# Optimization experiments

Hardware: AMD Instinct MI355X
Metric: run time of the kernel (lower is better)

The kernel has to match this reference:

```python
import jax, jax.numpy as jnp
import numpy as np

N = 262144
D_IN = 128
ENC_DIMS = [128, 512, 256, 64, 8]   # input -> hidden tanh layers -> linear latent
EST_DIMS = [8, 128, 64, 16]          # latent -> hidden tanh layers -> softmax K
EPS = 1e-6


def setup_inputs() -> dict:
    key = jax.random.key(0)
    ks = jax.random.split(key, 1 + 2 * (len(ENC_DIMS) - 1) + 2 * (len(EST_DIMS) - 1))
    it = iter(ks)
    inp = {"x": jax.random.normal(next(it), (N, D_IN), dtype=jnp.float32)}
    for i in range(len(ENC_DIMS) - 1):
        fan_in, fan_out = ENC_DIMS[i], ENC_DIMS[i + 1]
        inp[f"W{i}"] = jax.random.normal(next(it), (fan_in, fan_out), dtype=jnp.float32) * (1.0 / np.sqrt(fan_in))
        inp[f"b{i}"] = jnp.zeros((fan_out,), dtype=jnp.float32)
    for i in range(len(EST_DIMS) - 1):
        fan_in, fan_out = EST_DIMS[i], EST_DIMS[i + 1]
        inp[f"E{i}"] = jax.random.normal(next(it), (fan_in, fan_out), dtype=jnp.float32) * (1.0 / np.sqrt(fan_in))
        inp[f"eb{i}"] = jnp.zeros((fan_out,), dtype=jnp.float32)
    return inp


def _forward(x, W0, b0, W1, b1, W2, b2, W3, b3, E0, eb0, E1, eb1, E2, eb2):
    # CompressionNet encoder: tanh hidden layers, linear final
    h = jnp.tanh(x @ W0 + b0)
    h = jnp.tanh(h @ W1 + b1)
    h = jnp.tanh(h @ W2 + b2)
    z = h @ W3 + b3                                  # [N, d_z]

    # EstimationNet: tanh hidden layers, softmax final -> gamma [N, K]
    g = jnp.tanh(z @ E0 + eb0)
    g = jnp.tanh(g @ E1 + eb1)
    gamma = jax.nn.softmax(g @ E2 + eb2, axis=1)

    # GMM statistics
    gamma_sum = jnp.sum(gamma, axis=0)               # [K]
    phi = jnp.mean(gamma, axis=0)                    # [K]
    mu = (gamma.T @ z) / gamma_sum[:, None]          # [K, d_z]
    zc_raw = z[:, None, :] - mu[None, :, :]          # [N, K, d_z]
    zc = jnp.sqrt(gamma)[:, :, None] * zc_raw        # [N, K, d_z]
    sigma = jnp.einsum('nkl,nkm->klm', zc, zc) / gamma_sum[:, None, None]  # [K, d, d]
    d_z = z.shape[1]
    L = jnp.linalg.cholesky(sigma + EPS * jnp.eye(d_z, dtype=sigma.dtype)[None])

    # Energy: solve L v = (z - mu)^T per component, [K, d, N]
    v = jax.scipy.linalg.solve_triangular(L, jnp.transpose(zc_raw, (1, 2, 0)), lower=True)
    log_det_sigma = 2.0 * jnp.sum(jnp.log(jnp.diagonal(L, axis1=1, axis2=2)), axis=1)  # [K]
    logits = (jnp.log(phi)[:, None]
              - 0.5 * (jnp.sum(v * v, axis=1)
                       + d_z * jnp.log(2.0 * jnp.pi)
                       + log_det_sigma[:, None]))    # [K, N]
    prob = -jax.scipy.special.logsumexp(logits, axis=0)  # [N]
    return prob, z


def reference(x, W0, b0, W1, b1, W2, b2, W3, b3, E0, eb0, E1, eb1, E2, eb2):
    return _forward(x, W0, b0, W1, b1, W2, b2, W3, b3, E0, eb0, E1, eb1, E2, eb2)
```

## Files before the change

### kernel.cpp

```cpp
#include <hip/hip_runtime.h>
#include <math.h>

#define NSAMP 262144
#define TMS 64

typedef __bf16  bf16x8 __attribute__((ext_vector_type(8)));
typedef __bf16  bf16x4 __attribute__((ext_vector_type(4)));
typedef float   f32x4  __attribute__((ext_vector_type(4)));

__device__ __forceinline__ float fast_tanh(float v) {
  float e = __expf(2.0f * v);
  return 1.0f - 2.0f * __builtin_amdgcn_rcpf(e + 1.0f);
}
__device__ __forceinline__ unsigned short f2bf(float f) {
  unsigned u = __float_as_uint(f);
  unsigned r = (u + 0x7FFFu + ((u >> 16) & 1u)) >> 16;
  return (unsigned short)r;
}

__global__ void k0_pack(const float* __restrict__ W0, const float* __restrict__ W1,
                        const float* __restrict__ W2, const float* __restrict__ E1w,
                        const float* __restrict__ E0w, const float* __restrict__ W3,
                        const float* __restrict__ E2w,
                        unsigned short* __restrict__ wpack)
{
  const int f = blockIdx.x;
  const int lane = threadIdx.x;
  const float* W; int NKS, N, Kreal, Nreal, local;
  if (f < 128)      { W = W0;  NKS = 4;  N = 512; Kreal = 128; Nreal = 512; local = f; }
  else if (f < 384) { W = W1;  NKS = 16; N = 256; Kreal = 512; Nreal = 256; local = f - 128; }
  else if (f < 416) { W = W2;  NKS = 8;  N = 64;  Kreal = 256; Nreal = 64;  local = f - 384; }
  else if (f < 432) { W = E1w; NKS = 4;  N = 64;  Kreal = 128; Nreal = 64;  local = f - 416; }
  else if (f < 440) { W = E0w; NKS = 1;  N = 128; Kreal = 8;   Nreal = 128; local = f - 432; }
  else if (f < 442) { W = W3;  NKS = 2;  N = 8;   Kreal = 64;  Nreal = 8;   local = f - 440; }
  else              { W = E2w; NKS = 2;  N = 16;  Kreal = 64;  Nreal = 16;  local = f - 442; }
  const int nt = local / NKS, ks = local % NKS;
  const int n = nt * 16 + (lane & 15);
  const int kbase = ks * 32 + (lane >> 4) * 8;
  unsigned short* out = wpack + ((size_t)f * 64 + lane) * 8;
#pragma unroll
  for (int i = 0; i < 8; ++i) {
    const int k = kbase + i;
    const float v = (k < Kreal && n < Nreal) ? W[(size_t)k * N + n] : 0.f;
    out[i] = f2bf(v);
  }
}

template<int NTPW>
__device__ __forceinline__ void layer_nks4(
    const char* __restrict__ in, int inRowB, char* __restrict__ outb, int outRowB,
    const unsigned short* __restrict__ wp, int fragBase,
    const float* __restrict__ bias, int lane, int wv)
{
  const int l15 = lane & 15, lg = lane >> 4;
  const int sw = (l15 & 7) << 4;
  bf16x8 a[4][4];
#pragma unroll
  for (int sg = 0; sg < 4; ++sg)
#pragma unroll
    for (int q = 0; q < 4; ++q)
      a[sg][q] = *(const bf16x8*)(in + (sg * 16 + l15) * inRowB + ((q * 64 + lg * 16) ^ sw));
#pragma unroll
  for (int t = 0; t < NTPW; ++t) {
    const int nt = wv * NTPW + t;
    const float4 bv = *(const float4*)(bias + nt * 16 + lg * 4);
    f32x4 acc[4];
#pragma unroll
    for (int sg = 0; sg < 4; ++sg) acc[sg] = {bv.x, bv.y, bv.z, bv.w};
#pragma unroll
    for (int q = 0; q < 4; ++q) {
      const bf16x8 w = *(const bf16x8*)(wp + ((size_t)(fragBase + nt * 4 + q) * 64 + lane) * 8);
#pragma unroll
      for (int sg = 0; sg < 4; ++sg)
        acc[sg] = __builtin_amdgcn_mfma_f32_16x16x32_bf16(w, a[sg][q], acc[sg], 0, 0, 0);
    }
#pragma unroll
    for (int sg = 0; sg < 4; ++sg) {
      bf16x4 tv;
#pragma unroll
      for (int r = 0; r < 4; ++r) tv[r] = (__bf16)fast_tanh(acc[sg][r]);
      *(bf16x4*)(outb + (sg * 16 + l15) * outRowB + ((nt * 32 + lg * 8) ^ sw)) = tv;
    }
  }
}

template<int NCH>
__device__ __forceinline__ void l2_accum(
    const char* __restrict__ H1, const unsigned short* __restrict__ wp,
    int ksOff, f32x4 (&acc)[4][4], int lane, int wv)
{
  const int l15 = lane & 15, lg = lane >> 4;
  const int sw = (l15 & 7) << 4;
#pragma unroll
  for (int ch = 0; ch < NCH; ++ch) {
    bf16x8 a[4][4];
#pragma unroll
    for (int sg = 0; sg < 4; ++sg)
#pragma unroll
      for (int q = 0; q < 4; ++q)
        a[sg][q] = *(const bf16x8*)(H1 + (sg * 16 + l15) * 512 + (((ch * 4 + q) * 64 + lg * 16) ^ sw));
#pragma unroll
    for (int t = 0; t < 4; ++t) {
      const int nt = wv * 4 + t;
#pragma unroll
      for (int q = 0; q < 4; ++q) {
        const bf16x8 w = *(const bf16x8*)(wp + ((size_t)(128 + nt * 16 + ksOff + ch * 4 + q) * 64 + lane) * 8);
#pragma unroll
        for (int sg = 0; sg < 4; ++sg)
          acc[t][sg] = __builtin_amdgcn_mfma_f32_16x16x32_bf16(w, a[sg][q], acc[t][sg], 0, 0, 0);
      }
    }
  }
}

__global__ __launch_bounds__(256, 2) void k1_mfma(
    const float* __restrict__ x, const unsigned short* __restrict__ wpack,
    const float* __restrict__ b0, const float* __restrict__ b1,
    const float* __restrict__ b2, const float* __restrict__ b3,
    const float* __restrict__ eb0, const float* __restrict__ eb1,
    const float* __restrict__ eb2,
    float* __restrict__ zg, float* __restrict__ gamma)
{
  __shared__ char sm[81920];
  char* H1  = sm;
  char* H2  = sm + 32768;
  char* X   = sm + 65536;
  char* L3o = sm + 65536;
  char* zb  = sm + 73728;
  char* E0o = sm;
  char* e1  = sm + 32768;

  const int tid = threadIdx.x;
  const int lane = tid & 63, wv = tid >> 6;
  const int l15 = lane & 15, lg = lane >> 4;
  const int sw = (l15 & 7) << 4;
  const int blk = blockIdx.x;

  {
    const float* xb = x + (size_t)blk * (TMS * 128);
#pragma unroll
    for (int p = 0; p < 8; ++p) {
      const int v = tid + p * 256;
      const float4 t = *(const float4*)(xb + v * 4);
      const int s = v >> 5, k0 = (v & 31) * 4;
      bf16x4 h = {(__bf16)t.x, (__bf16)t.y, (__bf16)t.z, (__bf16)t.w};
      *(bf16x4*)(X + s * 256 + ((k0 * 2) ^ ((s & 7) << 4))) = h;
    }
  }

  f32x4 acc2[4][4];
#pragma unroll
  for (int t = 0; t < 4; ++t) {
    const float4 bv = *(const float4*)(b1 + (wv * 4 + t) * 16 + lg * 4);
#pragma unroll
    for (int sg = 0; sg < 4; ++sg) acc2[t][sg] = {bv.x, bv.y, bv.z, bv.w};
  }
  __syncthreads();

  layer_nks4<4>(X, 256, H1, 512, wpack, 0, b0, lane, wv);
  __syncthreads();
  l2_accum<2>(H1, wpack, 0, acc2, lane, wv);
  __syncthreads();
  layer_nks4<4>(X, 256, H1, 512, wpack, 64, b0 + 256, lane, wv);
  __syncthreads();
  l2_accum<2>(H1, wpack, 8, acc2, lane, wv);

#pragma unroll
  for (int t = 0; t < 4; ++t)
#pragma unroll
    for (int sg = 0; sg < 4; ++sg) {
      bf16x4 tv;
#pragma unroll
      for (int r = 0; r < 4; ++r) tv[r] = (__bf16)fast_tanh(acc2[t][sg][r]);
      *(bf16x4*)(H2 + (sg * 16 + l15) * 512 + (((wv * 4 + t) * 32 + lg * 8) ^ sw)) = tv;
    }
  __syncthreads();

  {
    f32x4 acc[4];
    const float4 bv = *(const float4*)(b2 + wv * 16 + lg * 4);
#pragma unroll
    for (int sg = 0; sg < 4; ++sg) acc[sg] = {bv.x, bv.y, bv.z, bv.w};
#pragma unroll
    for (int ch = 0; ch < 2; ++ch) {
      bf16x8 a[4][4];
#pragma unroll
      for (int sg = 0; sg < 4; ++sg)
#pragma unroll
        for (int q = 0; q < 4; ++q)
          a[sg][q] = *(const bf16x8*)(H2 + (sg * 16 + l15) * 512 + (((ch * 4 + q) * 64 + lg * 16) ^ sw));
#pragma unroll
      for (int q = 0; q < 4; ++q) {
        const bf16x8 w = *(const bf16x8*)(wpack + ((size_t)(384 + wv * 8 + ch * 4 + q) * 64 + lane) * 8);
#pragma unroll
        for (int sg = 0; sg < 4; ++sg)
          acc[sg] = __builtin_amdgcn_mfma_f32_16x16x32_bf16(w, a[sg][q], acc[sg], 0, 0, 0);
      }
    }
#pragma unroll
    for (int sg = 0; sg < 4; ++sg) {
      bf16x4 tv;
#pragma unroll
      for (int r = 0; r < 4; ++r) tv[r] = (__bf16)fast_tanh(acc[sg][r]);
      *(bf16x4*)(L3o + (sg * 16 + l15) * 128 + ((wv * 32 + lg * 8) ^ sw)) = tv;
    }
  }
  __syncthreads();

  {
    bf16x8 a[2];
#pragma unroll
    for (int q = 0; q < 2; ++q)
      a[q] = *(const bf16x8*)(L3o + (wv * 16 + l15) * 128 + ((q * 64 + lg * 16) ^ sw));
    float4 bv = {0.f, 0.f, 0.f, 0.f};
    if (lg < 2) bv = *(const float4*)(b3 + lg * 4);
    f32x4 acc = {bv.x, bv.y, bv.z, bv.w};
#pragma unroll
    for (int q = 0; q < 2; ++q) {
      const bf16x8 w = *(const bf16x8*)(wpack + ((size_t)(440 + q) * 64 + lane) * 8);
      acc = __builtin_amdgcn_mfma_f32_16x16x32_bf16(w, a[q], acc, 0, 0, 0);
    }
    if (lg < 2) {
      *(f32x4*)(zg + ((size_t)blk * 64 + wv * 16 + l15) * 8 + lg * 4) = acc;
      bf16x4 zv;
#pragma unroll
      for (int r = 0; r < 4; ++r) zv[r] = (__bf16)acc[r];
      *(bf16x4*)(zb + (wv * 16 + l15) * 16 + lg * 8) = zv;
    }
  }
  __syncthreads();

  {
    bf16x8 az[4];
#pragma unroll
    for (int sg = 0; sg < 4; ++sg)
      az[sg] = *(const bf16x8*)(zb + (sg * 16 + l15) * 16);
#pragma unroll
    for (int t = 0; t < 2; ++t) {
      const int nt = wv * 2 + t;
      const float4 bv = *(const float4*)(eb0 + nt * 16 + lg * 4);
      const bf16x8 w = *(const bf16x8*)(wpack + ((size_t)(432 + nt) * 64 + lane) * 8);
#pragma unroll
      for (int sg = 0; sg < 4; ++sg) {
        f32x4 acc = {bv.x, bv.y, bv.z, bv.w};
        acc = __builtin_amdgcn_mfma_f32_16x16x32_bf16(w, az[sg], acc, 0, 0, 0);
        bf16x4 tv;
#pragma unroll
        for (int r = 0; r < 4; ++r) tv[r] = (__bf16)fast_tanh(acc[r]);
        *(bf16x4*)(E0o + (sg * 16 + l15) * 256 + ((nt * 32 + lg * 8) ^ sw)) = tv;
      }
    }
  }
  __syncthreads();

  layer_nks4<1>(E0o, 256, e1, 128, wpack, 416, eb1, lane, wv);
  __syncthreads();

  {
    bf16x8 a[2];
#pragma unroll
    for (int q = 0; q < 2; ++q)
      a[q] = *(const bf16x8*)(e1 + (wv * 16 + l15) * 128 + ((q * 64 + lg * 16) ^ sw));
    const float4 bv = *(const float4*)(eb2 + lg * 4);
    f32x4 acc = {bv.x, bv.y, bv.z, bv.w};
#pragma unroll
    for (int q = 0; q < 2; ++q) {
      const bf16x8 w = *(const bf16x8*)(wpack + ((size_t)(442 + q) * 64 + lane) * 8);
      acc = __builtin_amdgcn_mfma_f32_16x16x32_bf16(w, a[q], acc, 0, 0, 0);
    }
    float m = fmaxf(fmaxf(acc[0], acc[1]), fmaxf(acc[2], acc[3]));
    m = fmaxf(m, __shfl_xor(m, 16));
    m = fmaxf(m, __shfl_xor(m, 32));
    float e0v = __expf(acc[0] - m), e1v = __expf(acc[1] - m);
    float e2v = __expf(acc[2] - m), e3v = __expf(acc[3] - m);
    float s = e0v + e1v + e2v + e3v;
    s += __shfl_xor(s, 16);
    s += __shfl_xor(s, 32);
    const float inv = __builtin_amdgcn_rcpf(s);
    float4 g = {e0v * inv, e1v * inv, e2v * inv, e3v * inv};
    *(float4*)(gamma + ((size_t)blk * 64 + wv * 16 + l15) * 16 + lg * 4) = g;
  }
}

__global__ __launch_bounds__(256) void k2a_partial(
    const float* __restrict__ zg, const float* __restrict__ gamma,
    float* __restrict__ part)
{
  __shared__ float zl[256 * 8];
  __shared__ float gl[256 * 16];
  __shared__ float red[4][16][46];
  const int tid = threadIdx.x;
  const int blk = blockIdx.x;
  const int s0 = blk * 256;

  {
    const float4 a = *(const float4*)(zg + (size_t)(s0 + tid) * 8);
    const float4 b = *(const float4*)(zg + (size_t)(s0 + tid) * 8 + 4);
    *(float4*)(&zl[tid * 8])     = a;
    *(float4*)(&zl[tid * 8 + 4]) = b;
  }
  {
    const float* gp = gamma + (size_t)(s0 + tid) * 16;
#pragma unroll
    for (int q = 0; q < 4; ++q)
      *(float4*)(&gl[tid * 16 + q * 4]) = *(const float4*)(gp + q * 4);
  }
  __syncthreads();

  const int k = tid & 15, sub = tid >> 4;
  float m2[36], m1[8], gs = 0.f;
#pragma unroll
  for (int i = 0; i < 36; ++i) m2[i] = 0.f;
#pragma unroll
  for (int i = 0; i < 8; ++i) m1[i] = 0.f;

#pragma unroll 4
  for (int i = 0; i < 16; ++i) {
    const int n = i * 16 + sub;
    const float4 za = *(const float4*)(&zl[n * 8]);
    const float4 zb4 = *(const float4*)(&zl[n * 8 + 4]);
    const float zv[8] = {za.x, za.y, za.z, za.w, zb4.x, zb4.y, zb4.z, zb4.w};
    const float g = gl[n * 16 + k];
    gs += g;
    float t[8];
#pragma unroll
    for (int l = 0; l < 8; ++l) { t[l] = g * zv[l]; m1[l] += t[l]; }
    int p = 0;
#pragma unroll
    for (int l = 0; l < 8; ++l)
#pragma unroll
      for (int m = l; m < 8; ++m) {
        m2[p] = fmaf(t[l], zv[m], m2[p]);
        ++p;
      }
  }

#pragma unroll
  for (int i = 0; i < 36; ++i) {
    m2[i] += __shfl_xor(m2[i], 16);
    m2[i] += __shfl_xor(m2[i], 32);
  }
#pragma unroll
  for (int i = 0; i < 8; ++i) {
    m1[i] += __shfl_xor(m1[i], 16);
    m1[i] += __shfl_xor(m1[i], 32);
  }
  gs += __shfl_xor(gs, 16);
  gs += __shfl_xor(gs, 32);

  const int lane = tid & 63, wv = tid >> 6;
  if (lane < 16) {
#pragma unroll
    for (int i = 0; i < 36; ++i) red[wv][lane][i] = m2[i];
#pragma unroll
    for (int i = 0; i < 8; ++i) red[wv][lane][36 + i] = m1[i];
    red[wv][lane][44] = gs;
  }
  __syncthreads();

  for (int o = tid; o < 768; o += 256) {
    const int kk = o / 48, p = o % 48;
    float v = 0.f;
    if (p < 45)
      v = red[0][kk][p] + red[1][kk][p] + red[2][kk][p] + red[3][kk][p];
    part[(size_t)blk * 768 + o] = v;
  }
}

__global__ __launch_bounds__(256) void k2b_reduce(
    const float* __restrict__ part, float* __restrict__ stats)
{
  const int oi = blockIdx.x % 3, jc = blockIdx.x / 3;
  const int o = oi * 256 + threadIdx.x;
  float s = 0.f;
#pragma unroll 4
  for (int j = jc * 128; j < jc * 128 + 128; ++j)
    s += part[(size_t)j * 768 + o];
  atomicAdd(&stats[o], s);
}

__global__ void k3_finalize(const float* __restrict__ stats, float* __restrict__ coef)
{
  const int k = threadIdx.x;
  if (k >= 16) return;
  const float* sk = stats + k * 48;
  const float gs = sk[44];
  float mu[8];
#pragma unroll
  for (int l = 0; l < 8; ++l) mu[l] = sk[36 + l] / gs;

  float S[8][8];
  {
    int p = 0;
    for (int l = 0; l < 8; ++l)
      for (int m = l; m < 8; ++m) {
        const float v = sk[p++] / gs - mu[l] * mu[m];
        S[l][m] = v; S[m][l] = v;
      }
  }
  for (int l = 0; l < 8; ++l) S[l][l] += 1e-6f;

  float L[8][8];
  for (int i = 0; i < 8; ++i)
    for (int j = 0; j <= i; ++j) {
      float s = S[i][j];
      for (int t = 0; t < j; ++t) s -= L[i][t] * L[j][t];
      if (i == j) L[i][i] = sqrtf(s);
      else        L[i][j] = s / L[j][j];
    }
  float logdet = 0.f;
  for (int i = 0; i < 8; ++i) logdet += logf(L[i][i]);
  logdet *= 2.f;

  float U[8][8];
  for (int j = 0; j < 8; ++j) {
    U[j][j] = 1.f / L[j][j];
    for (int i = j + 1; i < 8; ++i) {
      float s = 0.f;
      for (int t = j; t < i; ++t) s += L[i][t] * U[t][j];
      U[i][j] = -s / L[i][i];
    }
  }
  float Amat[8][8];
  for (int l = 0; l < 8; ++l)
    for (int m = l; m < 8; ++m) {
      float s = 0.f;
      for (int i = m; i < 8; ++i) s += U[i][l] * U[i][m];
      Amat[l][m] = s; Amat[m][l] = s;
    }
  float c[8];
  for (int l = 0; l < 8; ++l) {
    float s = 0.f;
    for (int m = 0; m < 8; ++m) s += Amat[l][m] * mu[m];
    c[l] = s;
  }
  float muAmu = 0.f;
  for (int l = 0; l < 8; ++l) muAmu += c[l] * mu[l];

  const float LOG2PI = 1.8378770664093453f;
  const float cnst = logf(gs) - logf((float)NSAMP)
                   - 0.5f * (8.f * LOG2PI + logdet + muAmu);

  float* ck = coef + k * 48;
  {
    int p = 0;
    for (int l = 0; l < 8; ++l)
      for (int m = l; m < 8; ++m) {
        ck[p] = (l == m) ? (-0.5f * Amat[l][l]) : (-Amat[l][m]);
        ++p;
      }
  }
  for (int l = 0; l < 8; ++l) ck[36 + l] = c[l];
  ck[44] = cnst;
  ck[45] = 0.f; ck[46] = 0.f; ck[47] = 0.f;
}

__global__ __launch_bounds__(256) void k4_energy(
    const float* __restrict__ zg, const float* __restrict__ coef,
    float* __restrict__ prob)
{
  __shared__ float C[16 * 48];
  for (int i = threadIdx.x; i < 16 * 48; i += 256) C[i] = coef[i];
  __syncthreads();

  const int n = blockIdx.x * 256 + threadIdx.x;
  const float4 za = *(const float4*)(zg + (size_t)n * 8);
  const float4 zb = *(const float4*)(zg + (size_t)n * 8 + 4);
  const float z[8] = {za.x, za.y, za.z, za.w, zb.x, zb.y, zb.z, zb.w};

  float pr[36];
  {
    int p = 0;
#pragma unroll
    for (int l = 0; l < 8; ++l)
#pragma unroll
      for (int m = l; m < 8; ++m) pr[p++] = z[l] * z[m];
  }

  float mx = -1e30f, sm = 0.f;
#pragma unroll
  for (int k = 0; k < 16; ++k) {
    const float4* c4 = (const float4*)&C[k * 48];
    float acc = C[k * 48 + 44];
#pragma unroll
    for (int q = 0; q < 9; ++q) {
      const float4 t = c4[q];
      acc = fmaf(t.x, pr[q * 4 + 0], acc);
      acc = fmaf(t.y, pr[q * 4 + 1], acc);
      acc = fmaf(t.z, pr[q * 4 + 2], acc);
      acc = fmaf(t.w, pr[q * 4 + 3], acc);
    }
    {
      const float4 t = c4[9];
      acc = fmaf(t.x, z[0], acc); acc = fmaf(t.y, z[1], acc);
      acc = fmaf(t.z, z[2], acc); acc = fmaf(t.w, z[3], acc);
    }
    {
      const float4 t = c4[10];
      acc = fmaf(t.x, z[4], acc); acc = fmaf(t.y, z[5], acc);
      acc = fmaf(t.z, z[6], acc); acc = fmaf(t.w, z[7], acc);
    }
    const float nm = fmaxf(mx, acc);
    sm = sm * __expf(mx - nm) + __expf(acc - nm);
    mx = nm;
  }
  prob[n] = -(mx + __logf(sm));
}

extern "C" void kernel_launch(void* const* d_in, const int* in_sizes, int n_in,
                              void* d_out, int out_size, void* d_ws, size_t ws_size,
                              hipStream_t stream)
{
  const float* x   = (const float*)d_in[0];
  const float* W0  = (const float*)d_in[1];
  const float* b0  = (const float*)d_in[2];
  const float* W1  = (const float*)d_in[3];
  const float* b1  = (const float*)d_in[4];
  const float* W2  = (const float*)d_in[5];
  const float* b2  = (const float*)d_in[6];
  const float* W3  = (const float*)d_in[7];
  const float* b3  = (const float*)d_in[8];
  const float* E0w = (const float*)d_in[9];
  const float* eb0 = (const float*)d_in[10];
  const float* E1w = (const float*)d_in[11];
  const float* eb1 = (const float*)d_in[12];
  const float* E2w = (const float*)d_in[13];
  const float* eb2 = (const float*)d_in[14];

  float* out  = (float*)d_out;
  float* prob = out;
  float* zg   = out + NSAMP;

  unsigned short* wpack = (unsigned short*)d_ws;
  float* ws    = (float*)d_ws;
  float* gamma = ws + 114688;
  float* stats = gamma + (size_t)NSAMP * 16;
  float* coef  = stats + 768;
  float* part  = coef + 768;

  hipMemsetAsync(stats, 0, 768 * sizeof(float), stream);

  k0_pack<<<444, 64, 0, stream>>>(W0, W1, W2, E1w, E0w, W3, E2w, wpack);
  k1_mfma<<<NSAMP / TMS, 256, 0, stream>>>(x, wpack, b0, b1, b2, b3,
                                           eb0, eb1, eb2, zg, gamma);
  k2a_partial<<<1024, 256, 0, stream>>>(zg, gamma, part);
  k2b_reduce<<<24, 256, 0, stream>>>(part, stats);
  k3_finalize<<<1, 64, 0, stream>>>(stats, coef);
  k4_energy<<<NSAMP / 256, 256, 0, stream>>>(zg, coef, prob);
}
```

Before: 204.4 us.

## Fuse GMM partial statistics into MLP kernel and shrink shared memory footprint

The per-sample gamma write and the separate k2a_partial kernel are removed. Each k1 block now reduces the GMM moment statistics for its 64 samples in shared memory and writes partials directly. Layer 1/2 processing is split into four 128-wide chunks and layer 3 into two halves, cutting LDS use from 80KB to 48KB so occupancy can rise to 3 blocks per CU. This saves a 16MB gamma round trip and one launch. In exchange, k2b now reduces four times more partials, and k1 has more barriers and higher register pressure.

Measured after the change: 301.8 us. 1.48x slower.

```diff
diff --git a/kernel.cpp b/kernel.cpp
--- a/kernel.cpp
+++ b/kernel.cpp
@@ -84,51 +84,67 @@
   }
 }
 
-template<int NCH>
-__device__ __forceinline__ void l2_accum(
+__device__ __forceinline__ void l2_accum_q(
     const char* __restrict__ H1, const unsigned short* __restrict__ wp,
     int ksOff, f32x4 (&acc)[4][4], int lane, int wv)
 {
   const int l15 = lane & 15, lg = lane >> 4;
   const int sw = (l15 & 7) << 4;
-#pragma unroll
-  for (int ch = 0; ch < NCH; ++ch) {
-    bf16x8 a[4][4];
-#pragma unroll
-    for (int sg = 0; sg < 4; ++sg)
-#pragma unroll
-      for (int q = 0; q < 4; ++q)
-        a[sg][q] = *(const bf16x8*)(H1 + (sg * 16 + l15) * 512 + (((ch * 4 + q) * 64 + lg * 16) ^ sw));
-#pragma unroll
-    for (int t = 0; t < 4; ++t) {
-      const int nt = wv * 4 + t;
-#pragma unroll
-      for (int q = 0; q < 4; ++q) {
-        const bf16x8 w = *(const bf16x8*)(wp + ((size_t)(128 + nt * 16 + ksOff + ch * 4 + q) * 64 + lane) * 8);
-#pragma unroll
-        for (int sg = 0; sg < 4; ++sg)
-          acc[t][sg] = __builtin_amdgcn_mfma_f32_16x16x32_bf16(w, a[sg][q], acc[t][sg], 0, 0, 0);
-      }
-    }
-  }
-}
-
-__global__ __launch_bounds__(256, 2) void k1_mfma(
+  bf16x8 a[4][4];
+#pragma unroll
+  for (int sg = 0; sg < 4; ++sg)
+#pragma unroll
+    for (int q = 0; q < 4; ++q)
+      a[sg][q] = *(const bf16x8*)(H1 + (sg * 16 + l15) * 256 + ((q * 64 + lg * 16) ^ sw));
+#pragma unroll
+  for (int t = 0; t < 4; ++t) {
+    const int nt = wv * 4 + t;
+#pragma unroll
+    for (int q = 0; q < 4; ++q) {
+      const bf16x8 w = *(const bf16x8*)(wp + ((size_t)(128 + nt * 16 + ksOff + q) * 64 + lane) * 8);
+#pragma unroll
+      for (int sg = 0; sg < 4; ++sg)
+        acc[t][sg] = __builtin_amdgcn_mfma_f32_16x16x32_bf16(w, a[sg][q], acc[t][sg], 0, 0, 0);
+    }
+  }
+}
+
+__device__ __forceinline__ void l3_accum_h(
+    const char* __restrict__ H2, const unsigned short* __restrict__ wp,
+    int ksOff, f32x4 (&acc)[4], int lane, int wv)
+{
+  const int l15 = lane & 15, lg = lane >> 4;
+  const int sw = (l15 & 7) << 4;
+#pragma unroll
+  for (int q = 0; q < 4; ++q) {
+    const bf16x8 w = *(const bf16x8*)(wp + ((size_t)(384 + wv * 8 + ksOff + q) * 64 + lane) * 8);
+#pragma unroll
+    for (int sg = 0; sg < 4; ++sg) {
+      const bf16x8 a = *(const bf16x8*)(H2 + (sg * 16 + l15) * 256 + ((q * 64 + lg * 16) ^ sw));
+      acc[sg] = __builtin_amdgcn_mfma_f32_16x16x32_bf16(w, a, acc[sg], 0, 0, 0);
+    }
+  }
+}
+
+__global__ __launch_bounds__(256, 3) void k1_mfma(
     const float* __restrict__ x, const unsigned short* __restrict__ wpack,
     const float* __restrict__ b0, const float* __restrict__ b1,
     const float* __restrict__ b2, const float* __restrict__ b3,
     const float* __restrict__ eb0, const float* __restrict__ eb1,
     const float* __restrict__ eb2,
-    float* __restrict__ zg, float* __restrict__ gamma)
-{
-  __shared__ char sm[81920];
-  char* H1  = sm;
+    float* __restrict__ zg, float* __restrict__ part)
+{
+  __shared__ char sm[49152];
+  char* X   = sm;
+  char* H1  = sm + 16384;
   char* H2  = sm + 32768;
-  char* X   = sm + 65536;
-  char* L3o = sm + 65536;
-  char* zb  = sm + 73728;
-  char* E0o = sm;
+  char* L3o = sm;
+  float* zf = (float*)(sm + 8192);
+  char* zb  = sm + 10240;
+  float* gl = (float*)(sm + 11264);
+  char* E0o = sm + 16384;
   char* e1  = sm + 32768;
+  float (*red)[16][46] = (float(*)[16][46])(sm + 16384);
 
   const int tid = threadIdx.x;
   const int lane = tid & 63, wv = tid >> 6;
@@ -157,53 +173,58 @@
   }
   __syncthreads();
 
-  layer_nks4<4>(X, 256, H1, 512, wpack, 0, b0, lane, wv);
-  __syncthreads();
-  l2_accum<2>(H1, wpack, 0, acc2, lane, wv);
-  __syncthreads();
-  layer_nks4<4>(X, 256, H1, 512, wpack, 64, b0 + 256, lane, wv);
-  __syncthreads();
-  l2_accum<2>(H1, wpack, 8, acc2, lane, wv);
-
-#pragma unroll
-  for (int t = 0; t < 4; ++t)
-#pragma unroll
-    for (int sg = 0; sg < 4; ++sg) {
-      bf16x4 tv;
-#pragma unroll
-      for (int r = 0; r < 4; ++r) tv[r] = (__bf16)fast_tanh(acc2[t][sg][r]);
-      *(bf16x4*)(H2 + (sg * 16 + l15) * 512 + (((wv * 4 + t) * 32 + lg * 8) ^ sw)) = tv;
-    }
-  __syncthreads();
-
-  {
-    f32x4 acc[4];
+#pragma unroll
+  for (int p = 0; p < 4; ++p) {
+    layer_nks4<2>(X, 256, H1, 256, wpack, p * 32, b0 + p * 128, lane, wv);
+    __syncthreads();
+    l2_accum_q(H1, wpack, p * 4, acc2, lane, wv);
+    __syncthreads();
+  }
+
+  f32x4 acc3[4];
+  {
     const float4 bv = *(const float4*)(b2 + wv * 16 + lg * 4);
 #pragma unroll
-    for (int sg = 0; sg < 4; ++sg) acc[sg] = {bv.x, bv.y, bv.z, bv.w};
-#pragma unroll
-    for (int ch = 0; ch < 2; ++ch) {
-      bf16x8 a[4][4];
-#pragma unroll
-      for (int sg = 0; sg < 4; ++sg)
-#pragma unroll
-        for (int q = 0; q < 4; ++q)
-          a[sg][q] = *(const bf16x8*)(H2 + (sg * 16 + l15) * 512 + (((ch * 4 + q) * 64 + lg * 16) ^ sw));
-#pragma unroll
-      for (int q = 0; q < 4; ++q) {
-        const bf16x8 w = *(const bf16x8*)(wpack + ((size_t)(384 + wv * 8 + ch * 4 + q) * 64 + lane) * 8);
-#pragma unroll
-        for (int sg = 0; sg < 4; ++sg)
-          acc[sg] = __builtin_amdgcn_mfma_f32_16x16x32_bf16(w, a[sg][q], acc[sg], 0, 0, 0);
+    for (int sg = 0; sg < 4; ++sg) acc3[sg] = {bv.x, bv.y, bv.z, bv.w};
+  }
+
+  if (wv < 2) {
+#pragma unroll
+    for (int t = 0; t < 4; ++t)
+#pragma unroll
+      for (int sg = 0; sg < 4; ++sg) {
+        bf16x4 tv;
+#pragma unroll
+        for (int r = 0; r < 4; ++r) tv[r] = (__bf16)fast_tanh(acc2[t][sg][r]);
+        const int tl = wv * 4 + t;
+        *(bf16x4*)(H2 + (sg * 16 + l15) * 256 + ((tl * 32 + lg * 8) ^ sw)) = tv;
       }
-    }
-#pragma unroll
-    for (int sg = 0; sg < 4; ++sg) {
-      bf16x4 tv;
-#pragma unroll
-      for (int r = 0; r < 4; ++r) tv[r] = (__bf16)fast_tanh(acc[sg][r]);
-      *(bf16x4*)(L3o + (sg * 16 + l15) * 128 + ((wv * 32 + lg * 8) ^ sw)) = tv;
-    }
+  }
+  __syncthreads();
+  l3_accum_h(H2, wpack, 0, acc3, lane, wv);
+  __syncthreads();
+
+  if (wv >= 2) {
+#pragma unroll
+    for (int t = 0; t < 4; ++t)
+#pragma unroll
+      for (int sg = 0; sg < 4; ++sg) {
+        bf16x4 tv;
+#pragma unroll
+        for (int r = 0; r < 4; ++r) tv[r] = (__bf16)fast_tanh(acc2[t][sg][r]);
+        const int tl = (wv - 2) * 4 + t;
+        *(bf16x4*)(H2 + (sg * 16 + l15) * 256 + ((tl * 32 + lg * 8) ^ sw)) = tv;
+      }
+  }
+  __syncthreads();
+  l3_accum_h(H2, wpack, 4, acc3, lane, wv);
+
+#pragma unroll
+  for (int sg = 0; sg < 4; ++sg) {
+    bf16x4 tv;
+#pragma unroll
+    for (int r = 0; r < 4; ++r) tv[r] = (__bf16)fast_tanh(acc3[sg][r]);
+    *(bf16x4*)(L3o + (sg * 16 + l15) * 128 + ((wv * 32 + lg * 8) ^ sw)) = tv;
   }
   __syncthreads();
 
@@ -222,6 +243,7 @@
     }
     if (lg < 2) {
       *(f32x4*)(zg + ((size_t)blk * 64 + wv * 16 + l15) * 8 + lg * 4) = acc;
+      *(f32x4*)(zf + (wv * 16 + l15) * 8 + lg * 4) = acc;
       bf16x4 zv;
 #pragma unroll
       for (int r = 0; r < 4; ++r) zv[r] = (__bf16)acc[r];
@@ -277,84 +299,57 @@
     s += __shfl_xor(s, 16);
     s += __shfl_xor(s, 32);
     const float inv = __builtin_amdgcn_rcpf(s);
-    float4 g = {e0v * inv, e1v * inv, e2v * inv, e3v * inv};
-    *(float4*)(gamma + ((size_t)blk * 64 + wv * 16 + l15) * 16 + lg * 4) = g;
-  }
-}
-
-__global__ __launch_bounds__(256) void k2a_partial(
-    const float* __restrict__ zg, const float* __restrict__ gamma,
-    float* __restrict__ part)
-{
-  __shared__ float zl[256 * 8];
-  __shared__ float gl[256 * 16];
-  __shared__ float red[4][16][46];
-  const int tid = threadIdx.x;
-  const int blk = blockIdx.x;
-  const int s0 = blk * 256;
-
-  {
-    const float4 a = *(const float4*)(zg + (size_t)(s0 + tid) * 8);
-    const float4 b = *(const float4*)(zg + (size_t)(s0 + tid) * 8 + 4);
-    *(float4*)(&zl[tid * 8])     = a;
-    *(float4*)(&zl[tid * 8 + 4]) = b;
-  }
-  {
-    const float* gp = gamma + (size_t)(s0 + tid) * 16;
-#pragma unroll
-    for (int q = 0; q < 4; ++q)
-      *(float4*)(&gl[tid * 16 + q * 4]) = *(const float4*)(gp + q * 4);
-  }
-  __syncthreads();
-
-  const int k = tid & 15, sub = tid >> 4;
-  float m2[36], m1[8], gs = 0.f;
-#pragma unroll
-  for (int i = 0; i < 36; ++i) m2[i] = 0.f;
-#pragma unroll
-  for (int i = 0; i < 8; ++i) m1[i] = 0.f;
-
-#pragma unroll 4
-  for (int i = 0; i < 16; ++i) {
-    const int n = i * 16 + sub;
-    const float4 za = *(const float4*)(&zl[n * 8]);
-    const float4 zb4 = *(const float4*)(&zl[n * 8 + 4]);
-    const float zv[8] = {za.x, za.y, za.z, za.w, zb4.x, zb4.y, zb4.z, zb4.w};
-    const float g = gl[n * 16 + k];
-    gs += g;
-    float t[8];
-#pragma unroll
-    for (int l = 0; l < 8; ++l) { t[l] = g * zv[l]; m1[l] += t[l]; }
-    int p = 0;
-#pragma unroll
-    for (int l = 0; l < 8; ++l)
-#pragma unroll
-      for (int m = l; m < 8; ++m) {
-        m2[p] = fmaf(t[l], zv[m], m2[p]);
-        ++p;
-      }
-  }
-
-#pragma unroll
-  for (int i = 0; i < 36; ++i) {
-    m2[i] += __shfl_xor(m2[i], 16);
-    m2[i] += __shfl_xor(m2[i], 32);
-  }
-#pragma unroll
-  for (int i = 0; i < 8; ++i) {
-    m1[i] += __shfl_xor(m1[i], 16);
-    m1[i] += __shfl_xor(m1[i], 32);
-  }
-  gs += __shfl_xor(gs, 16);
-  gs += __shfl_xor(gs, 32);
-
-  const int lane = tid & 63, wv = tid >> 6;
-  if (lane < 16) {
-#pragma unroll
-    for (int i = 0; i < 36; ++i) red[wv][lane][i] = m2[i];
-#pragma unroll
-    for (int i = 0; i < 8; ++i) red[wv][lane][36 + i] = m1[i];
-    red[wv][lane][44] = gs;
+    *(float4*)(gl + (wv * 16 + l15) * 16 + lg * 4) =
+        (float4){e0v * inv, e1v * inv, e2v * inv, e3v * inv};
+  }
+  __syncthreads();
+
+  {
+    const int kk = tid & 15, sub = tid >> 4;
+    float m2[36], m1[8], gs = 0.f;
+#pragma unroll
+    for (int i = 0; i < 36; ++i) m2[i] = 0.f;
+#pragma unroll
+    for (int i = 0; i < 8; ++i) m1[i] = 0.f;
+#pragma unroll
+    for (int i = 0; i < 4; ++i) {
+      const int n = sub * 4 + i;
+      const float4 za = *(const float4*)(zf + n * 8);
+      const float4 zc = *(const float4*)(zf + n * 8 + 4);
+      const float zv[8] = {za.x, za.y, za.z, za.w, zc.x, zc.y, zc.z, zc.w};
+      const float g = gl[n * 16 + kk];
+      gs += g;
+      float t[8];
+#pragma unroll
+      for (int l = 0; l < 8; ++l) { t[l] = g * zv[l]; m1[l] += t[l]; }
+      int p = 0;
+#pragma unroll
+      for (int l = 0; l < 8; ++l)
+#pragma unroll
+        for (int m = l; m < 8; ++m) {
+          m2[p] = fmaf(t[l], zv[m], m2[p]);
+          ++p;
+        }
+    }
+#pragma unroll
+    for (int i = 0; i < 36; ++i) {
+      m2[i] += __shfl_xor(m2[i], 16);
+      m2[i] += __shfl_xor(m2[i], 32);
+    }
+#pragma unroll
+    for (int i = 0; i < 8; ++i) {
+      m1[i] += __shfl_xor(m1[i], 16);
+      m1[i] += __shfl_xor(m1[i], 32);
+    }
+    gs += __shfl_xor(gs, 16);
+    gs += __shfl_xor(gs, 32);
+    if (lane < 16) {
+#pragma unroll
+      for (int i = 0; i < 36; ++i) red[wv][lane][i] = m2[i];
+#pragma unroll
+      for (int i = 0; i < 8; ++i) red[wv][lane][36 + i] = m1[i];
+      red[wv][lane][44] = gs;
+    }
   }
   __syncthreads();
 
@@ -374,7 +369,7 @@
   const int o = oi * 256 + threadIdx.x;
   float s = 0.f;
 #pragma unroll 4
-  for (int j = jc * 128; j < jc * 128 + 128; ++j)
+  for (int j = jc * 512; j < jc * 512 + 512; ++j)
     s += part[(size_t)j * 768 + o];
   atomicAdd(&stats[o], s);
 }
@@ -533,8 +528,7 @@
 
   unsigned short* wpack = (unsigned short*)d_ws;
   float* ws    = (float*)d_ws;
-  float* gamma = ws + 114688;
-  float* stats = gamma + (size_t)NSAMP * 16;
+  float* stats = ws + 114688;
   float* coef  = stats + 768;
   float* part  = coef + 768;
 
@@ -542,8 +536,7 @@
 
   k0_pack<<<444, 64, 0, stream>>>(W0, W1, W2, E1w, E0w, W3, E2w, wpack);
   k1_mfma<<<NSAMP / TMS, 256, 0, stream>>>(x, wpack, b0, b1, b2, b3,
-                                           eb0, eb1, eb2, zg, gamma);
-  k2a_partial<<<1024, 256, 0, stream>>>(zg, gamma, part);
+                                           eb0, eb1, eb2, zg, part);
   k2b_reduce<<<24, 256, 0, stream>>>(part, stats);
   k3_finalize<<<1, 64, 0, stream>>>(stats, coef);
   k4_energy<<<NSAMP / 256, 256, 0, stream>>>(zg, coef, prob);
```

## Fuse GMM moment partial sums into the MLP kernel, drop gamma buffer

Applied to the files above, without the earlier changes.

The per-block gamma-weighted first and second moment accumulation moves from a separate kernel into the end of the MLP kernel. Gamma and z stay in shared memory, so the 16 MB gamma array is no longer written and re-read, and one launch goes away. Partials are now one per 64-sample block (4096 instead of 1024), so the reduce kernel loops over 512 rows per block. This adds more partial traffic and reuses shared memory for the reduction scratch, which relies on earlier regions no longer being live.

After: 237.4 us. +16.1%, slower.

```diff
diff --git a/kernel.cpp b/kernel.cpp
--- a/kernel.cpp
+++ b/kernel.cpp
@@ -119,16 +119,19 @@
     const float* __restrict__ b2, const float* __restrict__ b3,
     const float* __restrict__ eb0, const float* __restrict__ eb1,
     const float* __restrict__ eb2,
-    float* __restrict__ zg, float* __restrict__ gamma)
+    float* __restrict__ zg, float* __restrict__ part)
 {
   __shared__ char sm[81920];
   char* H1  = sm;
   char* H2  = sm + 32768;
   char* X   = sm + 65536;
   char* L3o = sm + 65536;
-  char* zb  = sm + 73728;
+  float* zf = (float*)(sm + 73728);
+  char* zb  = sm + 75776;
+  float* gl = (float*)(sm + 76800);
   char* E0o = sm;
   char* e1  = sm + 32768;
+  float (*red)[16][46] = (float(*)[16][46])sm;
 
   const int tid = threadIdx.x;
   const int lane = tid & 63, wv = tid >> 6;
@@ -222,6 +225,7 @@
     }
     if (lg < 2) {
       *(f32x4*)(zg + ((size_t)blk * 64 + wv * 16 + l15) * 8 + lg * 4) = acc;
+      *(f32x4*)(zf + (wv * 16 + l15) * 8 + lg * 4) = acc;
       bf16x4 zv;
 #pragma unroll
       for (int r = 0; r < 4; ++r) zv[r] = (__bf16)acc[r];
@@ -277,84 +281,57 @@
     s += __shfl_xor(s, 16);
     s += __shfl_xor(s, 32);
     const float inv = __builtin_amdgcn_rcpf(s);
-    float4 g = {e0v * inv, e1v * inv, e2v * inv, e3v * inv};
-    *(float4*)(gamma + ((size_t)blk * 64 + wv * 16 + l15) * 16 + lg * 4) = g;
-  }
-}
-
-__global__ __launch_bounds__(256) void k2a_partial(
-    const float* __restrict__ zg, const float* __restrict__ gamma,
-    float* __restrict__ part)
-{
-  __shared__ float zl[256 * 8];
-  __shared__ float gl[256 * 16];
-  __shared__ float red[4][16][46];
-  const int tid = threadIdx.x;
-  const int blk = blockIdx.x;
-  const int s0 = blk * 256;
-
-  {
-    const float4 a = *(const float4*)(zg + (size_t)(s0 + tid) * 8);
-    const float4 b = *(const float4*)(zg + (size_t)(s0 + tid) * 8 + 4);
-    *(float4*)(&zl[tid * 8])     = a;
-    *(float4*)(&zl[tid * 8 + 4]) = b;
-  }
-  {
-    const float* gp = gamma + (size_t)(s0 + tid) * 16;
-#pragma unroll
-    for (int q = 0; q < 4; ++q)
-      *(float4*)(&gl[tid * 16 + q * 4]) = *(const float4*)(gp + q * 4);
-  }
-  __syncthreads();
-
-  const int k = tid & 15, sub = tid >> 4;
-  float m2[36], m1[8], gs = 0.f;
-#pragma unroll
-  for (int i = 0; i < 36; ++i) m2[i] = 0.f;
-#pragma unroll
-  for (int i = 0; i < 8; ++i) m1[i] = 0.f;
-
-#pragma unroll 4
-  for (int i = 0; i < 16; ++i) {
-    const int n = i * 16 + sub;
-    const float4 za = *(const float4*)(&zl[n * 8]);
-    const float4 zb4 = *(const float4*)(&zl[n * 8 + 4]);
-    const float zv[8] = {za.x, za.y, za.z, za.w, zb4.x, zb4.y, zb4.z, zb4.w};
-    const float g = gl[n * 16 + k];
-    gs += g;
-    float t[8];
-#pragma unroll
-    for (int l = 0; l < 8; ++l) { t[l] = g * zv[l]; m1[l] += t[l]; }
-    int p = 0;
-#pragma unroll
-    for (int l = 0; l < 8; ++l)
-#pragma unroll
-      for (int m = l; m < 8; ++m) {
-        m2[p] = fmaf(t[l], zv[m], m2[p]);
-        ++p;
-      }
-  }
-
-#pragma unroll
-  for (int i = 0; i < 36; ++i) {
-    m2[i] += __shfl_xor(m2[i], 16);
-    m2[i] += __shfl_xor(m2[i], 32);
-  }
-#pragma unroll
-  for (int i = 0; i < 8; ++i) {
-    m1[i] += __shfl_xor(m1[i], 16);
-    m1[i] += __shfl_xor(m1[i], 32);
-  }
-  gs += __shfl_xor(gs, 16);
-  gs += __shfl_xor(gs, 32);
-
-  const int lane = tid & 63, wv = tid >> 6;
-  if (lane < 16) {
-#pragma unroll
-    for (int i = 0; i < 36; ++i) red[wv][lane][i] = m2[i];
-#pragma unroll
-    for (int i = 0; i < 8; ++i) red[wv][lane][36 + i] = m1[i];
-    red[wv][lane][44] = gs;
+    *(float4*)(gl + (wv * 16 + l15) * 16 + lg * 4) =
+        (float4){e0v * inv, e1v * inv, e2v * inv, e3v * inv};
+  }
+  __syncthreads();
+
+  {
+    const int kk = tid & 15, sub = tid >> 4;
+    float m2[36], m1[8], gs = 0.f;
+#pragma unroll
+    for (int i = 0; i < 36; ++i) m2[i] = 0.f;
+#pragma unroll
+    for (int i = 0; i < 8; ++i) m1[i] = 0.f;
+#pragma unroll
+    for (int i = 0; i < 4; ++i) {
+      const int n = sub * 4 + i;
+      const float4 za = *(const float4*)(zf + n * 8);
+      const float4 zc = *(const float4*)(zf + n * 8 + 4);
+      const float zv[8] = {za.x, za.y, za.z, za.w, zc.x, zc.y, zc.z, zc.w};
+      const float g = gl[n * 16 + kk];
+      gs += g;
+      float t[8];
+#pragma unroll
+      for (int l = 0; l < 8; ++l) { t[l] = g * zv[l]; m1[l] += t[l]; }
+      int p = 0;
+#pragma unroll
+      for (int l = 0; l < 8; ++l)
+#pragma unroll
+        for (int m = l; m < 8; ++m) {
+          m2[p] = fmaf(t[l], zv[m], m2[p]);
+          ++p;
+        }
+    }
+#pragma unroll
+    for (int i = 0; i < 36; ++i) {
+      m2[i] += __shfl_xor(m2[i], 16);
+      m2[i] += __shfl_xor(m2[i], 32);
+    }
+#pragma unroll
+    for (int i = 0; i < 8; ++i) {
+      m1[i] += __shfl_xor(m1[i], 16);
+      m1[i] += __shfl_xor(m1[i], 32);
+    }
+    gs += __shfl_xor(gs, 16);
+    gs += __shfl_xor(gs, 32);
+    if (lane < 16) {
+#pragma unroll
+      for (int i = 0; i < 36; ++i) red[wv][lane][i] = m2[i];
+#pragma unroll
+      for (int i = 0; i < 8; ++i) red[wv][lane][36 + i] = m1[i];
+      red[wv][lane][44] = gs;
+    }
   }
   __syncthreads();
 
@@ -374,7 +351,7 @@
   const int o = oi * 256 + threadIdx.x;
   float s = 0.f;
 #pragma unroll 4
-  for (int j = jc * 128; j < jc * 128 + 128; ++j)
+  for (int j = jc * 512; j < jc * 512 + 512; ++j)
     s += part[(size_t)j * 768 + o];
   atomicAdd(&stats[o], s);
 }
@@ -533,8 +510,7 @@
 
   unsigned short* wpack = (unsigned short*)d_ws;
   float* ws    = (float*)d_ws;
-  float* gamma = ws + 114688;
-  float* stats = gamma + (size_t)NSAMP * 16;
+  float* stats = ws + 114688;
   float* coef  = stats + 768;
   float* part  = coef + 768;
 
@@ -542,8 +518,7 @@
 
   k0_pack<<<444, 64, 0, stream>>>(W0, W1, W2, E1w, E0w, W3, E2w, wpack);
   k1_mfma<<<NSAMP / TMS, 256, 0, stream>>>(x, wpack, b0, b1, b2, b3,
-                                           eb0, eb1, eb2, zg, gamma);
-  k2a_partial<<<1024, 256, 0, stream>>>(zg, gamma, part);
+                                           eb0, eb1, eb2, zg, part);
   k2b_reduce<<<24, 256, 0, stream>>>(part, stats);
   k3_finalize<<<1, 64, 0, stream>>>(stats, coef);
   k4_energy<<<NSAMP / 256, 256, 0, stream>>>(zg, coef, prob);
```

## Make tail layers wave-private by sample rows to drop block barriers

Applied to the files above, without the earlier changes.

The later narrow layers (W2, W3, E0, E1) now split work by sample rows instead of output columns. Each wave computes all output columns for its own 16 samples, so every LDS read hits data the same wave wrote, and several __syncthreads barriers are removed. Each wave now loads every weight tile instead of a quarter of them, so global/L2 weight traffic per wave goes up. The e1 buffer is moved to avoid overlapping E0o.

New measurement: 212.2 us. 1.04x slower.

```diff
diff --git a/kernel.cpp b/kernel.cpp
--- a/kernel.cpp
+++ b/kernel.cpp
@@ -128,7 +128,7 @@
   char* L3o = sm + 65536;
   char* zb  = sm + 73728;
   char* E0o = sm;
-  char* e1  = sm + 32768;
+  char* e1  = sm + 65536;
 
   const int tid = threadIdx.x;
   const int lane = tid & 63, wv = tid >> 6;
@@ -177,35 +177,34 @@
   __syncthreads();
 
   {
-    f32x4 acc[4];
-    const float4 bv = *(const float4*)(b2 + wv * 16 + lg * 4);
-#pragma unroll
-    for (int sg = 0; sg < 4; ++sg) acc[sg] = {bv.x, bv.y, bv.z, bv.w};
+    f32x4 acc3[4];
+#pragma unroll
+    for (int nt = 0; nt < 4; ++nt) {
+      const float4 bv = *(const float4*)(b2 + nt * 16 + lg * 4);
+      acc3[nt] = {bv.x, bv.y, bv.z, bv.w};
+    }
 #pragma unroll
     for (int ch = 0; ch < 2; ++ch) {
-      bf16x8 a[4][4];
-#pragma unroll
-      for (int sg = 0; sg < 4; ++sg)
-#pragma unroll
-        for (int q = 0; q < 4; ++q)
-          a[sg][q] = *(const bf16x8*)(H2 + (sg * 16 + l15) * 512 + (((ch * 4 + q) * 64 + lg * 16) ^ sw));
-#pragma unroll
-      for (int q = 0; q < 4; ++q) {
-        const bf16x8 w = *(const bf16x8*)(wpack + ((size_t)(384 + wv * 8 + ch * 4 + q) * 64 + lane) * 8);
-#pragma unroll
-        for (int sg = 0; sg < 4; ++sg)
-          acc[sg] = __builtin_amdgcn_mfma_f32_16x16x32_bf16(w, a[sg][q], acc[sg], 0, 0, 0);
-      }
-    }
-#pragma unroll
-    for (int sg = 0; sg < 4; ++sg) {
+      bf16x8 a[4];
+#pragma unroll
+      for (int q = 0; q < 4; ++q)
+        a[q] = *(const bf16x8*)(H2 + (wv * 16 + l15) * 512 + (((ch * 4 + q) * 64 + lg * 16) ^ sw));
+#pragma unroll
+      for (int nt = 0; nt < 4; ++nt)
+#pragma unroll
+        for (int q = 0; q < 4; ++q) {
+          const bf16x8 w = *(const bf16x8*)(wpack + ((size_t)(384 + nt * 8 + ch * 4 + q) * 64 + lane) * 8);
+          acc3[nt] = __builtin_amdgcn_mfma_f32_16x16x32_bf16(w, a[q], acc3[nt], 0, 0, 0);
+        }
+    }
+#pragma unroll
+    for (int nt = 0; nt < 4; ++nt) {
       bf16x4 tv;
 #pragma unroll
-      for (int r = 0; r < 4; ++r) tv[r] = (__bf16)fast_tanh(acc[sg][r]);
-      *(bf16x4*)(L3o + (sg * 16 + l15) * 128 + ((wv * 32 + lg * 8) ^ sw)) = tv;
-    }
-  }
-  __syncthreads();
+      for (int r = 0; r < 4; ++r) tv[r] = (__bf16)fast_tanh(acc3[nt][r]);
+      *(bf16x4*)(L3o + (wv * 16 + l15) * 128 + ((nt * 32 + lg * 8) ^ sw)) = tv;
+    }
+  }
 
   {
     bf16x8 a[2];
@@ -228,33 +227,42 @@
       *(bf16x4*)(zb + (wv * 16 + l15) * 16 + lg * 8) = zv;
     }
   }
-  __syncthreads();
-
-  {
-    bf16x8 az[4];
-#pragma unroll
-    for (int sg = 0; sg < 4; ++sg)
-      az[sg] = *(const bf16x8*)(zb + (sg * 16 + l15) * 16);
-#pragma unroll
-    for (int t = 0; t < 2; ++t) {
-      const int nt = wv * 2 + t;
+
+  {
+    const bf16x8 az = *(const bf16x8*)(zb + (wv * 16 + l15) * 16);
+#pragma unroll
+    for (int nt = 0; nt < 8; ++nt) {
       const float4 bv = *(const float4*)(eb0 + nt * 16 + lg * 4);
       const bf16x8 w = *(const bf16x8*)(wpack + ((size_t)(432 + nt) * 64 + lane) * 8);
-#pragma unroll
-      for (int sg = 0; sg < 4; ++sg) {
-        f32x4 acc = {bv.x, bv.y, bv.z, bv.w};
-        acc = __builtin_amdgcn_mfma_f32_16x16x32_bf16(w, az[sg], acc, 0, 0, 0);
-        bf16x4 tv;
-#pragma unroll
-        for (int r = 0; r < 4; ++r) tv[r] = (__bf16)fast_tanh(acc[r]);
-        *(bf16x4*)(E0o + (sg * 16 + l15) * 256 + ((nt * 32 + lg * 8) ^ sw)) = tv;
+      f32x4 acc = {bv.x, bv.y, bv.z, bv.w};
+      acc = __builtin_amdgcn_mfma_f32_16x16x32_bf16(w, az, acc, 0, 0, 0);
+      bf16x4 tv;
+#pragma unroll
+      for (int r = 0; r < 4; ++r) tv[r] = (__bf16)fast_tanh(acc[r]);
+      *(bf16x4*)(E0o + (wv * 16 + l15) * 256 + ((nt * 32 + lg * 8) ^ sw)) = tv;
+    }
+  }
+
+  {
+    bf16x8 a[4];
+#pragma unroll
+    for (int q = 0; q < 4; ++q)
+      a[q] = *(const bf16x8*)(E0o + (wv * 16 + l15) * 256 + ((q * 64 + lg * 16) ^ sw));
+#pragma unroll
+    for (int nt = 0; nt < 4; ++nt) {
+      const float4 bv = *(const float4*)(eb1 + nt * 16 + lg * 4);
+      f32x4 acc = {bv.x, bv.y, bv.z, bv.w};
+#pragma unroll
+      for (int q = 0; q < 4; ++q) {
+        const bf16x8 w = *(const bf16x8*)(wpack + ((size_t)(416 + nt * 4 + q) * 64 + lane) * 8);
+        acc = __builtin_amdgcn_mfma_f32_16x16x32_bf16(w, a[q], acc, 0, 0, 0);
       }
-    }
-  }
-  __syncthreads();
-
-  layer_nks4<1>(E0o, 256, e1, 128, wpack, 416, eb1, lane, wv);
-  __syncthreads();
+      bf16x4 tv;
+#pragma unroll
+      for (int r = 0; r < 4; ++r) tv[r] = (__bf16)fast_tanh(acc[r]);
+      *(bf16x4*)(e1 + (wv * 16 + l15) * 128 + ((nt * 32 + lg * 8) ^ sw)) = tv;
+    }
+  }
 
   {
     bf16x8 a[2];
```
